# Performance work log

Measured on AMD Instinct MI355X. Metric: run time of the kernel, lower is better.

The kernel has to match this reference:

```python
import jax, jax.numpy as jnp
import numpy as np

K, D, N, W, OUT = 16, 2, 16384, 256, 1
TW = 0.2  # fixed_transition_width


def setup_inputs() -> dict:
    key = jax.random.key(0)
    ks = jax.random.split(key, 9)
    # 4x4 grid of subdomains over [0,1]^2
    edges = np.linspace(0.0, 1.0, 5).astype(np.float32)
    mins = np.array([[edges[i], edges[j]] for i in range(4) for j in range(4)], np.float32)
    maxs = mins + 0.25

    def init_w(k, shape, fan_in):
        return jax.random.normal(k, shape, jnp.float32) / np.sqrt(fan_in).astype(np.float32)

    return {
        "x": jax.random.uniform(ks[0], (N, D), jnp.float32),
        "W0": init_w(ks[1], (K, D, W), D),
        "b0": jnp.zeros((K, W), jnp.float32),
        "W1": init_w(ks[2], (K, W, W), W),
        "b1": jnp.zeros((K, W), jnp.float32),
        "W2": init_w(ks[3], (K, W, W), W),
        "b2": jnp.zeros((K, W), jnp.float32),
        "W3": init_w(ks[4], (K, W, OUT), W),
        "b3": jnp.zeros((K, OUT), jnp.float32),
        "xmins": jnp.asarray(mins),
        "xmaxs": jnp.asarray(maxs),
    }


def _cosine_window(xmins, xmaxs, wmin, x):
    """Normalized cosine partition-of-unity weights. x:[N,D], xmins/xmaxs:[K,D] -> [N,K]."""
    # smooth ramp 0->1 over [xmin-w, xmin+w] and 1->0 over [xmax-w, xmax+w], per dim
    t_l = jnp.clip((x[None] - (xmins - wmin)[:, None]) / (2.0 * wmin), 0.0, 1.0)  # [K,N,D]
    t_r = jnp.clip(((xmaxs + wmin)[:, None] - x[None]) / (2.0 * wmin), 0.0, 1.0)
    w_raw = jnp.prod(0.25 * (1.0 - jnp.cos(jnp.pi * t_l)) * (1.0 - jnp.cos(jnp.pi * t_r)), axis=-1)  # [K,N]
    w = w_raw / (jnp.sum(w_raw, axis=0, keepdims=True) + 1e-9)
    return w.T  # [N,K]


def reference(x, W0, b0, W1, b1, W2, b2, W3, b3, xmins, xmaxs):
    all_w = _cosine_window(xmins, xmaxs, TW, x)  # [N,K]
    # per-subdomain normalization of x to [-1,1]
    center = (xmins + xmaxs) * 0.5
    scale = jnp.maximum((xmaxs - xmins) * 0.5, 1e-9)
    xn = (x[None] - center[:, None]) / scale[:, None]  # [K,N,D]
    # batched small MLPs (one per subdomain), tanh hidden activations
    h = jnp.tanh(jnp.einsum('knd,kdw->knw', xn, W0) + b0[:, None])
    h = jnp.tanh(jnp.einsum('knw,kwv->knv', h, W1) + b1[:, None])
    h = jnp.tanh(jnp.einsum('knw,kwv->knv', h, W2) + b2[:, None])
    sub = jnp.einsum('knw,kwo->kno', h, W3) + b3[:, None]  # [K,N,OUT]
    # window-weighted combine; ansatz is identity in the NN output
    return jnp.einsum('nk,kno->no', all_w, sub)  # [N,OUT]
```

## Files before the change

kernel.cpp:

```cpp
#include <hip/hip_runtime.h>
#include <stdint.h>

#define TWF 0.2f
#define NPTS 16384

typedef __attribute__((ext_vector_type(8))) short short8;
typedef __attribute__((ext_vector_type(4))) float floatx4;

__device__ __forceinline__ short f2bf(float f){
  unsigned u = __float_as_uint(f);
  u += 0x7fff + ((u >> 16) & 1);
  return (short)(u >> 16);
}
__device__ __forceinline__ float bf2f(short s){
  return __uint_as_float(((unsigned)(unsigned short)s) << 16);
}
__device__ __forceinline__ float fast_tanh(float x){
  float e = __builtin_amdgcn_exp2f(x * 2.885390082f);
  float r = __builtin_amdgcn_rcpf(e + 1.f);
  return fmaf(-2.f, r, 1.f);
}
__device__ __forceinline__ float cospi_t(float t){
  return __builtin_amdgcn_cosf(t * 0.5f);
}
__device__ __forceinline__ unsigned cvt_pk_bf16(float lo, float hi){
  unsigned r;
  asm("v_cvt_pk_bf16_f32 %0, %1, %2" : "=v"(r) : "v"(lo), "v"(hi));
  return r;
}

#define WS_W      0
#define WS_REC    (4u<<20)
#define WS_CNT    (8u<<20)
#define CNT(k)    counts[(k) * 32]

__global__ __launch_bounds__(256) void prep_fused(
    const float* __restrict__ W1, const float* __restrict__ W2,
    const float* __restrict__ x,  const float* __restrict__ xmins,
    const float* __restrict__ xmaxs, short* __restrict__ dst,
    int* __restrict__ counts, floatx4* __restrict__ rec,
    float* __restrict__ out){
  if (blockIdx.x < 1024){
    int gid = blockIdx.x * 256 + threadIdx.x;
    int lane = gid & 63; int rest = gid >> 6;
    int jt = rest & 15; rest >>= 4;
    int ks = rest & 7;  rest >>= 3;
    int k  = rest & 15; int mat = rest >> 4;
    const float* W = mat ? W2 : W1;
    int j   = jt * 16 + (lane & 15);
    int kk0 = ks * 32 + (lane >> 4) * 8;
    short8 v;
    #pragma unroll
    for (int jj = 0; jj < 8; jj++)
      v[jj] = f2bf(W[k * 65536 + (kk0 + jj) * 256 + j]);
    *(short8*)(dst + (size_t)gid * 8) = v;
  } else {
    __shared__ int s_wrt[4][4];
    __shared__ int s_base;
    int b2   = blockIdx.x - 1024;
    int k    = b2 & 15;
    int cb   = (b2 >> 4) * 1024;
    int t    = threadIdx.x;
    int lane = t & 63, wave = t >> 6;

    float cx  = (xmins[k * 2 + 0] + xmaxs[k * 2 + 0]) * 0.5f;
    float cy  = (xmins[k * 2 + 1] + xmaxs[k * 2 + 1]) * 0.5f;
    float sxi = 1.f / fmaxf((xmaxs[k * 2 + 0] - xmins[k * 2 + 0]) * 0.5f, 1e-9f);
    float syi = 1.f / fmaxf((xmaxs[k * 2 + 1] - xmins[k * 2 + 1]) * 0.5f, 1e-9f);

    float pxr[4], pyr[4], sum[4], wk[4];
    #pragma unroll
    for (int r = 0; r < 4; r++){
      int p = cb + r * 256 + t;
      float2 xy = *(const float2*)&x[p * 2];
      pxr[r] = xy.x; pyr[r] = xy.y; sum[r] = 0.f; wk[r] = 0.f;
      if (k == 0) out[p] = 0.f;
    }
    #pragma unroll
    for (int kk = 0; kk < 16; kk++){
      float mnx = xmins[kk * 2 + 0], mny = xmins[kk * 2 + 1];
      float mxx = xmaxs[kk * 2 + 0], mxy = xmaxs[kk * 2 + 1];
      #pragma unroll
      for (int r = 0; r < 4; r++){
        float tlx = fminf(fmaxf((pxr[r] - (mnx - TWF)) * (1.f/(2.f*TWF)), 0.f), 1.f);
        float trx = fminf(fmaxf(((mxx + TWF) - pxr[r]) * (1.f/(2.f*TWF)), 0.f), 1.f);
        float tly = fminf(fmaxf((pyr[r] - (mny - TWF)) * (1.f/(2.f*TWF)), 0.f), 1.f);
        float tr2 = fminf(fmaxf(((mxy + TWF) - pyr[r]) * (1.f/(2.f*TWF)), 0.f), 1.f);
        float wx = 0.25f * (1.f - cospi_t(tlx)) * (1.f - cospi_t(trx));
        float wy = 0.25f * (1.f - cospi_t(tly)) * (1.f - cospi_t(tr2));
        float w  = wx * wy;
        sum[r] += w;
        if (kk == k) wk[r] = w;
      }
    }
    bool act[4]; float wn[4], xa[4], xb[4];
    unsigned long long msk[4]; int wtot[4];
    #pragma unroll
    for (int r = 0; r < 4; r++){
      float inv = 1.f / (sum[r] + 1e-9f);
      act[r] = wk[r] > 0.f;
      wn[r]  = wk[r] * inv;
      xa[r]  = (pxr[r] - cx) * sxi;
      xb[r]  = (pyr[r] - cy) * syi;
      msk[r] = __ballot(act[r]);
      wtot[r] = (int)__popcll(msk[r]);
    }
    if (lane == 0){
      #pragma unroll
      for (int r = 0; r < 4; r++) s_wrt[wave][r] = wtot[r];
    }
    __syncthreads();
    int wavebase = 0, blocktot = 0;
    #pragma unroll
    for (int w = 0; w < 4; w++){
      int ws_ = s_wrt[w][0] + s_wrt[w][1] + s_wrt[w][2] + s_wrt[w][3];
      blocktot += ws_;
      wavebase += (w < wave) ? ws_ : 0;
    }
    if (t == 0) s_base = atomicAdd(&CNT(k), blocktot);
    __syncthreads();
    int rb = 0;
    #pragma unroll
    for (int r = 0; r < 4; r++){
      if (act[r]){
        int pos = s_base + wavebase + rb +
                  (int)__popcll(msk[r] & ((1ull << lane) - 1ull));
        int p = cb + r * 256 + t;
        rec[k * NPTS + pos] = (floatx4){xa[r], xb[r], wn[r], __int_as_float(p)};
      }
      rb += s_wrt[wave][r];
    }
  }
}

__device__ __forceinline__ void store_h_packed(
    short* lds_h, const floatx4 (&acc)[4][4], const floatx4 (&bb)[4],
    int wave, int quad, int col){
  #pragma unroll
  for (int rt = 0; rt < 4; rt++){
    const int j0    = (wave * 4 + rt) * 16 + quad * 4;
    const int cbase = j0 >> 3;
    const int off   = j0 & 7;
    #pragma unroll
    for (int ct = 0; ct < 4; ct++){
      const int m = ct * 16 + col;
      float t0 = fast_tanh(acc[rt][ct][0] + bb[rt][0]);
      float t1 = fast_tanh(acc[rt][ct][1] + bb[rt][1]);
      float t2 = fast_tanh(acc[rt][ct][2] + bb[rt][2]);
      float t3 = fast_tanh(acc[rt][ct][3] + bb[rt][3]);
      uint2 v = make_uint2(cvt_pk_bf16(t0, t1), cvt_pk_bf16(t2, t3));
      *(uint2*)&lds_h[m * 256 + ((cbase ^ (m & 7)) << 3) + off] = v;
    }
  }
}

__global__ __launch_bounds__(256, 4) void fbpinn_main(
    const float* __restrict__ W0, const float* __restrict__ b0,
    const float* __restrict__ b1, const float* __restrict__ b2,
    const float* __restrict__ W3, const float* __restrict__ b3,
    const short* __restrict__ wsw, const int* __restrict__ counts,
    const floatx4* __restrict__ rec, float* __restrict__ out)
{
  __shared__ short lds_h[64 * 256];
  __shared__ float s_xn[64 * 2];
  __shared__ float s_win[64];
  __shared__ int   s_pidx[64];
  __shared__ float s_w3[256];
  __shared__ float s_w0[512];

  const int t    = threadIdx.x;
  const int lane = t & 63;
  const int wave = t >> 6;
  const int col  = lane & 15;
  const int quad = lane >> 4;

  int tb[17]; tb[0] = 0;
  #pragma unroll
  for (int kk = 0; kk < 16; kk++) tb[kk + 1] = tb[kk] + ((CNT(kk) + 63) >> 6);
  const int total = tb[16];

  const int xcd   = blockIdx.x & 7;
  const int nb    = gridDim.x >> 3;
  const int chunk = (total + 7) >> 3;

  for (int idx = blockIdx.x >> 3; idx < chunk; idx += nb){
    const int tile = xcd * chunk + idx;
    if (tile >= total) break;
    int k = 0;
    #pragma unroll
    for (int kk = 1; kk < 16; kk++) k += (tile >= tb[kk]);
    const int base = (tile - tb[k]) * 64;
    const int cnt  = CNT(k);

    __syncthreads();

    s_w3[t] = W3[k * 256 + t];
    s_w0[t] = W0[k * 512 + t];
    s_w0[256 + t] = W0[k * 512 + 256 + t];
    if (t < 64){
      int gi = base + t;
      bool valid = gi < cnt;
      floatx4 rc = rec[k * NPTS + (valid ? gi : 0)];
      s_pidx[t] = __float_as_int(rc[3]);
      s_win[t]  = valid ? rc[2] : 0.f;
      s_xn[t * 2 + 0] = rc[0];
      s_xn[t * 2 + 1] = rc[1];
    }
    __syncthreads();

    {
      short8 wfr[4], xfr[4];
      #pragma unroll
      for (int rt = 0; rt < 4; rt++){
        int j = (wave * 4 + rt) * 16 + col;
        short8 a;
        #pragma unroll
        for (int i = 0; i < 8; i++) a[i] = 0;
        a[0] = (quad == 0) ? f2bf(s_w0[j])       : (short)0;
        a[1] = (quad == 0) ? f2bf(s_w0[256 + j]) : (short)0;
        wfr[rt] = a;
      }
      #pragma unroll
      for (int ct = 0; ct < 4; ct++){
        int m = ct * 16 + col;
        short8 b;
        #pragma unroll
        for (int i = 0; i < 8; i++) b[i] = 0;
        b[0] = (quad == 0) ? f2bf(s_xn[m * 2 + 0]) : (short)0;
        b[1] = (quad == 0) ? f2bf(s_xn[m * 2 + 1]) : (short)0;
        xfr[ct] = b;
      }
      floatx4 bb[4];
      #pragma unroll
      for (int rt = 0; rt < 4; rt++)
        bb[rt] = *(const floatx4*)&b0[k * 256 + (wave * 4 + rt) * 16 + quad * 4];
      floatx4 acc[4][4];
      #pragma unroll
      for (int a = 0; a < 4; a++)
        #pragma unroll
        for (int b = 0; b < 4; b++)
          acc[a][b] = (floatx4){0.f, 0.f, 0.f, 0.f};
      #pragma unroll
      for (int rt = 0; rt < 4; rt++)
        #pragma unroll
        for (int ct = 0; ct < 4; ct++)
          acc[rt][ct] = __builtin_amdgcn_mfma_f32_16x16x32_bf16(wfr[rt], xfr[ct], acc[rt][ct], 0, 0, 0);
      store_h_packed(lds_h, acc, bb, wave, quad, col);
      __syncthreads();
    }

    #pragma unroll 1
    for (int layer = 0; layer < 2; layer++){
      const short8* wb = (const short8*)(wsw + (size_t)layer * 1048576)
                         + ((size_t)(k * 8) * 16 + wave * 4) * 64 + lane;
      const float*  bp = layer ? b2 : b1;
      floatx4 bb[4];
      #pragma unroll
      for (int rt = 0; rt < 4; rt++)
        bb[rt] = *(const floatx4*)&bp[k * 256 + (wave * 4 + rt) * 16 + quad * 4];
      floatx4 acc[4][4];
      #pragma unroll
      for (int a = 0; a < 4; a++)
        #pragma unroll
        for (int b = 0; b < 4; b++)
          acc[a][b] = (floatx4){0.f, 0.f, 0.f, 0.f};

      short8 wcur[4];
      #pragma unroll
      for (int rt = 0; rt < 4; rt++) wcur[rt] = wb[rt * 64];

      #pragma unroll
      for (int ks = 0; ks < 8; ks++){
        short8 wnxt[4];
        if (ks < 7){
          #pragma unroll
          for (int rt = 0; rt < 4; rt++)
            wnxt[rt] = wb[(ks + 1) * 1024 + rt * 64];
        }
        short8 hfr[4];
        #pragma unroll
        for (int ct = 0; ct < 4; ct++){
          int m   = ct * 16 + col;
          int pos = (ks * 4 + quad) ^ (m & 7);
          hfr[ct] = *(const short8*)&lds_h[m * 256 + pos * 8];
        }
        #pragma unroll
        for (int rt = 0; rt < 4; rt++)
          #pragma unroll
          for (int ct = 0; ct < 4; ct++)
            acc[rt][ct] = __builtin_amdgcn_mfma_f32_16x16x32_bf16(wcur[rt], hfr[ct], acc[rt][ct], 0, 0, 0);
        if (ks < 7){
          #pragma unroll
          for (int rt = 0; rt < 4; rt++) wcur[rt] = wnxt[rt];
        }
      }
      __syncthreads();

      store_h_packed(lds_h, acc, bb, wave, quad, col);
      __syncthreads();
    }

    {
      int m = t >> 2, q = t & 3;
      float dot = 0.f;
      #pragma unroll
      for (int cc = 0; cc < 8; cc++){
        int ci  = q * 8 + cc;
        int pos = ci ^ (m & 7);
        short8 hv = *(const short8*)&lds_h[m * 256 + pos * 8];
        #pragma unroll
        for (int jj = 0; jj < 8; jj++)
          dot = fmaf(bf2f(hv[jj]), s_w3[ci * 8 + jj], dot);
      }
      dot += __shfl_xor(dot, 1);
      dot += __shfl_xor(dot, 2);
      if (q == 0 && s_win[m] != 0.f)
        atomicAdd(&out[s_pidx[m]], s_win[m] * (dot + b3[k]));
    }
  }
}

extern "C" void kernel_launch(void* const* d_in, const int* in_sizes, int n_in,
                              void* d_out, int out_size, void* d_ws, size_t ws_size,
                              hipStream_t stream){
  const float* x     = (const float*)d_in[0];
  const float* W0    = (const float*)d_in[1];
  const float* b0    = (const float*)d_in[2];
  const float* W1    = (const float*)d_in[3];
  const float* b1    = (const float*)d_in[4];
  const float* W2    = (const float*)d_in[5];
  const float* b2    = (const float*)d_in[6];
  const float* W3    = (const float*)d_in[7];
  const float* b3    = (const float*)d_in[8];
  const float* xmins = (const float*)d_in[9];
  const float* xmaxs = (const float*)d_in[10];
  float* out = (float*)d_out;

  char* ws = (char*)d_ws;
  short*   wsw  = (short*)  (ws + WS_W);
  floatx4* rc   = (floatx4*)(ws + WS_REC);
  int*     cnts = (int*)    (ws + WS_CNT);

  (void)hipMemsetAsync(cnts, 0, 4096, stream);
  prep_fused<<<1024 + 256, 256, 0, stream>>>(W1, W2, x, xmins, xmaxs,
                                             wsw, cnts, rc, out);
  fbpinn_main<<<1024, 256, 0, stream>>>(W0, b0, b1, b2, W3, b3,
                                        wsw, cnts, rc, out);
}
```

Baseline: 148.1 us.

## Replace atomic counters and memset with per-chunk counts and in-kernel scan

The prep kernel now writes compaction counts per (subdomain, 1024-point chunk) segment without atomics. The separate memset launch goes away, and the window computation is folded into every fourth block of the weight-conversion grid. The main kernel builds a 256-entry prefix scan in LDS and binary-searches it to map each tile to its segment. This removes one launch and the global atomics. In exchange it adds partially filled tiles per chunk, which means more padded MFMA work, plus a scan and search in every block.

```diff
diff --git a/kernel.cpp b/kernel.cpp
--- a/kernel.cpp
+++ b/kernel.cpp
@@ -32,16 +32,28 @@
 #define WS_W      0
 #define WS_REC    (4u<<20)
 #define WS_CNT    (8u<<20)
-#define CNT(k)    counts[(k) * 32]
-
-__global__ __launch_bounds__(256) void prep_fused(
+
+struct SMem {
+  short lds_h[64 * 256];
+  float s_xn[64 * 2];
+  float s_win[64];
+  int   s_pidx[64];
+  float s_w3[256];
+  float s_w0[512];
+  int   s_stb[257];
+  int   s_c[256];
+};
+
+__global__ __launch_bounds__(256) void fbpinn_p0(
     const float* __restrict__ W1, const float* __restrict__ W2,
     const float* __restrict__ x,  const float* __restrict__ xmins,
     const float* __restrict__ xmaxs, short* __restrict__ dst,
-    int* __restrict__ counts, floatx4* __restrict__ rec,
-    float* __restrict__ out){
-  if (blockIdx.x < 1024){
-    int gid = blockIdx.x * 256 + threadIdx.x;
+    int* __restrict__ cnt, floatx4* __restrict__ rec, float* __restrict__ out)
+{
+  __shared__ int s_wrt[16];
+  const int bid = blockIdx.x, t = threadIdx.x;
+  int gid = bid * 256 + t;
+  {
     int lane = gid & 63; int rest = gid >> 6;
     int jt = rest & 15; rest >>= 4;
     int ks = rest & 7;  rest >>= 3;
@@ -54,82 +66,78 @@
     for (int jj = 0; jj < 8; jj++)
       v[jj] = f2bf(W[k * 65536 + (kk0 + jj) * 256 + j]);
     *(short8*)(dst + (size_t)gid * 8) = v;
-  } else {
-    __shared__ int s_wrt[4][4];
-    __shared__ int s_base;
-    int b2   = blockIdx.x - 1024;
-    int k    = b2 & 15;
-    int cb   = (b2 >> 4) * 1024;
-    int t    = threadIdx.x;
-    int lane = t & 63, wave = t >> 6;
-
-    float cx  = (xmins[k * 2 + 0] + xmaxs[k * 2 + 0]) * 0.5f;
-    float cy  = (xmins[k * 2 + 1] + xmaxs[k * 2 + 1]) * 0.5f;
-    float sxi = 1.f / fmaxf((xmaxs[k * 2 + 0] - xmins[k * 2 + 0]) * 0.5f, 1e-9f);
-    float syi = 1.f / fmaxf((xmaxs[k * 2 + 1] - xmins[k * 2 + 1]) * 0.5f, 1e-9f);
-
-    float pxr[4], pyr[4], sum[4], wk[4];
+  }
+  if (gid < NPTS) out[gid] = 0.f;
+
+  if ((bid & 3) != 0) return;
+  int L  = bid >> 2;
+  int k  = L & 15, ch = L >> 4;
+  int cb = ch * 1024;
+  int lane = t & 63, wave = t >> 6;
+
+  float cx  = (xmins[k * 2 + 0] + xmaxs[k * 2 + 0]) * 0.5f;
+  float cy  = (xmins[k * 2 + 1] + xmaxs[k * 2 + 1]) * 0.5f;
+  float sxi = 1.f / fmaxf((xmaxs[k * 2 + 0] - xmins[k * 2 + 0]) * 0.5f, 1e-9f);
+  float syi = 1.f / fmaxf((xmaxs[k * 2 + 1] - xmins[k * 2 + 1]) * 0.5f, 1e-9f);
+
+  float pxr[4], pyr[4], sum[4], wk[4];
+  #pragma unroll
+  for (int r = 0; r < 4; r++){
+    int p = cb + r * 256 + t;
+    float2 xy = *(const float2*)&x[p * 2];
+    pxr[r] = xy.x; pyr[r] = xy.y; sum[r] = 0.f; wk[r] = 0.f;
+  }
+  #pragma unroll
+  for (int kk = 0; kk < 16; kk++){
+    float mnx = xmins[kk * 2 + 0], mny = xmins[kk * 2 + 1];
+    float mxx = xmaxs[kk * 2 + 0], mxy = xmaxs[kk * 2 + 1];
     #pragma unroll
     for (int r = 0; r < 4; r++){
+      float tlx = fminf(fmaxf((pxr[r] - (mnx - TWF)) * (1.f/(2.f*TWF)), 0.f), 1.f);
+      float trx = fminf(fmaxf(((mxx + TWF) - pxr[r]) * (1.f/(2.f*TWF)), 0.f), 1.f);
+      float tly = fminf(fmaxf((pyr[r] - (mny - TWF)) * (1.f/(2.f*TWF)), 0.f), 1.f);
+      float tr2 = fminf(fmaxf(((mxy + TWF) - pyr[r]) * (1.f/(2.f*TWF)), 0.f), 1.f);
+      float wx = 0.25f * (1.f - cospi_t(tlx)) * (1.f - cospi_t(trx));
+      float wy = 0.25f * (1.f - cospi_t(tly)) * (1.f - cospi_t(tr2));
+      float w  = wx * wy;
+      sum[r] += w;
+      if (kk == k) wk[r] = w;
+    }
+  }
+  bool act[4]; float wn[4], xa[4], xb[4];
+  unsigned long long msk[4]; int wtot[4];
+  #pragma unroll
+  for (int r = 0; r < 4; r++){
+    float inv = 1.f / (sum[r] + 1e-9f);
+    act[r] = wk[r] > 0.f;
+    wn[r]  = wk[r] * inv;
+    xa[r]  = (pxr[r] - cx) * sxi;
+    xb[r]  = (pyr[r] - cy) * syi;
+    msk[r] = __ballot(act[r]);
+    wtot[r] = (int)__popcll(msk[r]);
+  }
+  if (lane == 0){
+    #pragma unroll
+    for (int r = 0; r < 4; r++) s_wrt[wave * 4 + r] = wtot[r];
+  }
+  __syncthreads();
+  int wavebase = 0, blocktot = 0;
+  #pragma unroll
+  for (int w = 0; w < 4; w++){
+    int ws_ = s_wrt[w*4+0] + s_wrt[w*4+1] + s_wrt[w*4+2] + s_wrt[w*4+3];
+    blocktot += ws_;
+    wavebase += (w < wave) ? ws_ : 0;
+  }
+  if (t == 0) cnt[k * 16 + ch] = blocktot;
+  int rb = 0;
+  #pragma unroll
+  for (int r = 0; r < 4; r++){
+    if (act[r]){
+      int pos = wavebase + rb + (int)__popcll(msk[r] & ((1ull << lane) - 1ull));
       int p = cb + r * 256 + t;
-      float2 xy = *(const float2*)&x[p * 2];
-      pxr[r] = xy.x; pyr[r] = xy.y; sum[r] = 0.f; wk[r] = 0.f;
-      if (k == 0) out[p] = 0.f;
-    }
-    #pragma unroll
-    for (int kk = 0; kk < 16; kk++){
-      float mnx = xmins[kk * 2 + 0], mny = xmins[kk * 2 + 1];
-      float mxx = xmaxs[kk * 2 + 0], mxy = xmaxs[kk * 2 + 1];
-      #pragma unroll
-      for (int r = 0; r < 4; r++){
-        float tlx = fminf(fmaxf((pxr[r] - (mnx - TWF)) * (1.f/(2.f*TWF)), 0.f), 1.f);
-        float trx = fminf(fmaxf(((mxx + TWF) - pxr[r]) * (1.f/(2.f*TWF)), 0.f), 1.f);
-        float tly = fminf(fmaxf((pyr[r] - (mny - TWF)) * (1.f/(2.f*TWF)), 0.f), 1.f);
-        float tr2 = fminf(fmaxf(((mxy + TWF) - pyr[r]) * (1.f/(2.f*TWF)), 0.f), 1.f);
-        float wx = 0.25f * (1.f - cospi_t(tlx)) * (1.f - cospi_t(trx));
-        float wy = 0.25f * (1.f - cospi_t(tly)) * (1.f - cospi_t(tr2));
-        float w  = wx * wy;
-        sum[r] += w;
-        if (kk == k) wk[r] = w;
-      }
-    }
-    bool act[4]; float wn[4], xa[4], xb[4];
-    unsigned long long msk[4]; int wtot[4];
-    #pragma unroll
-    for (int r = 0; r < 4; r++){
-      float inv = 1.f / (sum[r] + 1e-9f);
-      act[r] = wk[r] > 0.f;
-      wn[r]  = wk[r] * inv;
-      xa[r]  = (pxr[r] - cx) * sxi;
-      xb[r]  = (pyr[r] - cy) * syi;
-      msk[r] = __ballot(act[r]);
-      wtot[r] = (int)__popcll(msk[r]);
-    }
-    if (lane == 0){
-      #pragma unroll
-      for (int r = 0; r < 4; r++) s_wrt[wave][r] = wtot[r];
-    }
-    __syncthreads();
-    int wavebase = 0, blocktot = 0;
-    #pragma unroll
-    for (int w = 0; w < 4; w++){
-      int ws_ = s_wrt[w][0] + s_wrt[w][1] + s_wrt[w][2] + s_wrt[w][3];
-      blocktot += ws_;
-      wavebase += (w < wave) ? ws_ : 0;
-    }
-    if (t == 0) s_base = atomicAdd(&CNT(k), blocktot);
-    __syncthreads();
-    int rb = 0;
-    #pragma unroll
-    for (int r = 0; r < 4; r++){
-      if (act[r]){
-        int pos = s_base + wavebase + rb +
-                  (int)__popcll(msk[r] & ((1ull << lane) - 1ull));
-        int p = cb + r * 256 + t;
-        rec[k * NPTS + pos] = (floatx4){xa[r], xb[r], wn[r], __int_as_float(p)};
-      }
-      rb += s_wrt[wave][r];
-    }
+      rec[k * NPTS + cb + pos] = (floatx4){xa[r], xb[r], wn[r], __int_as_float(p)};
+    }
+    rb += s_wrt[wave * 4 + r];
   }
 }
 
@@ -154,57 +162,64 @@
   }
 }
 
-__global__ __launch_bounds__(256, 4) void fbpinn_main(
+__global__ __launch_bounds__(256, 4) void fbpinn_p1(
     const float* __restrict__ W0, const float* __restrict__ b0,
     const float* __restrict__ b1, const float* __restrict__ b2,
     const float* __restrict__ W3, const float* __restrict__ b3,
-    const short* __restrict__ wsw, const int* __restrict__ counts,
+    const short* __restrict__ wsw, const int* __restrict__ cnt,
     const floatx4* __restrict__ rec, float* __restrict__ out)
 {
-  __shared__ short lds_h[64 * 256];
-  __shared__ float s_xn[64 * 2];
-  __shared__ float s_win[64];
-  __shared__ int   s_pidx[64];
-  __shared__ float s_w3[256];
-  __shared__ float s_w0[512];
-
-  const int t    = threadIdx.x;
+  __shared__ SMem sm;
+  const int bid  = blockIdx.x, t = threadIdx.x;
   const int lane = t & 63;
   const int wave = t >> 6;
   const int col  = lane & 15;
   const int quad = lane >> 4;
 
-  int tb[17]; tb[0] = 0;
-  #pragma unroll
-  for (int kk = 0; kk < 16; kk++) tb[kk + 1] = tb[kk] + ((CNT(kk) + 63) >> 6);
-  const int total = tb[16];
-
-  const int xcd   = blockIdx.x & 7;
-  const int nb    = gridDim.x >> 3;
-  const int chunk = (total + 7) >> 3;
-
-  for (int idx = blockIdx.x >> 3; idx < chunk; idx += nb){
-    const int tile = xcd * chunk + idx;
+  int* s_scan = (int*)sm.lds_h;
+  if (t < 256){ int c = cnt[t]; sm.s_c[t] = c; s_scan[t] = (c + 63) >> 6; }
+  __syncthreads();
+  for (int off = 1; off < 256; off <<= 1){
+    int v = (t >= off) ? s_scan[t - off] : 0;
+    __syncthreads();
+    s_scan[t] += v;
+    __syncthreads();
+  }
+  if (t < 256) sm.s_stb[t + 1] = s_scan[t];
+  if (t == 0)  sm.s_stb[0] = 0;
+  __syncthreads();
+  const int total = sm.s_stb[256];
+
+  const int xcd    = bid & 7;
+  const int nb     = gridDim.x >> 3;
+  const int chunkT = (total + 7) >> 3;
+
+  for (int idx = bid >> 3; idx < chunkT; idx += nb){
+    const int tile = xcd * chunkT + idx;
     if (tile >= total) break;
-    int k = 0;
-    #pragma unroll
-    for (int kk = 1; kk < 16; kk++) k += (tile >= tb[kk]);
-    const int base = (tile - tb[k]) * 64;
-    const int cnt  = CNT(k);
+    int lo = 0, hi = 256;
+    while (hi - lo > 1){
+      int mid = (lo + hi) >> 1;
+      if (tile >= sm.s_stb[mid]) lo = mid; else hi = mid;
+    }
+    const int seg = lo, k = seg >> 4, ch = seg & 15;
+    const int c     = sm.s_c[seg];
+    const int lbase = (tile - sm.s_stb[seg]) * 64;
+    const floatx4* rbase = rec + k * NPTS + ch * 1024;
 
     __syncthreads();
 
-    s_w3[t] = W3[k * 256 + t];
-    s_w0[t] = W0[k * 512 + t];
-    s_w0[256 + t] = W0[k * 512 + 256 + t];
+    sm.s_w3[t] = W3[k * 256 + t];
+    sm.s_w0[t] = W0[k * 512 + t];
+    sm.s_w0[256 + t] = W0[k * 512 + 256 + t];
     if (t < 64){
-      int gi = base + t;
-      bool valid = gi < cnt;
-      floatx4 rc = rec[k * NPTS + (valid ? gi : 0)];
-      s_pidx[t] = __float_as_int(rc[3]);
-      s_win[t]  = valid ? rc[2] : 0.f;
-      s_xn[t * 2 + 0] = rc[0];
-      s_xn[t * 2 + 1] = rc[1];
+      int li = lbase + t;
+      bool valid = li < c;
+      floatx4 rcd = rbase[valid ? li : 0];
+      sm.s_pidx[t] = __float_as_int(rcd[3]);
+      sm.s_win[t]  = valid ? rcd[2] : 0.f;
+      sm.s_xn[t * 2 + 0] = rcd[0];
+      sm.s_xn[t * 2 + 1] = rcd[1];
     }
     __syncthreads();
 
@@ -216,8 +231,8 @@
         short8 a;
         #pragma unroll
         for (int i = 0; i < 8; i++) a[i] = 0;
-        a[0] = (quad == 0) ? f2bf(s_w0[j])       : (short)0;
-        a[1] = (quad == 0) ? f2bf(s_w0[256 + j]) : (short)0;
+        a[0] = (quad == 0) ? f2bf(sm.s_w0[j])       : (short)0;
+        a[1] = (quad == 0) ? f2bf(sm.s_w0[256 + j]) : (short)0;
         wfr[rt] = a;
       }
       #pragma unroll
@@ -226,8 +241,8 @@
         short8 b;
         #pragma unroll
         for (int i = 0; i < 8; i++) b[i] = 0;
-        b[0] = (quad == 0) ? f2bf(s_xn[m * 2 + 0]) : (short)0;
-        b[1] = (quad == 0) ? f2bf(s_xn[m * 2 + 1]) : (short)0;
+        b[0] = (quad == 0) ? f2bf(sm.s_xn[m * 2 + 0]) : (short)0;
+        b[1] = (quad == 0) ? f2bf(sm.s_xn[m * 2 + 1]) : (short)0;
         xfr[ct] = b;
       }
       floatx4 bb[4];
@@ -245,7 +260,7 @@
         #pragma unroll
         for (int ct = 0; ct < 4; ct++)
           acc[rt][ct] = __builtin_amdgcn_mfma_f32_16x16x32_bf16(wfr[rt], xfr[ct], acc[rt][ct], 0, 0, 0);
-      store_h_packed(lds_h, acc, bb, wave, quad, col);
+      store_h_packed(sm.lds_h, acc, bb, wave, quad, col);
       __syncthreads();
     }
 
@@ -282,7 +297,7 @@
         for (int ct = 0; ct < 4; ct++){
           int m   = ct * 16 + col;
           int pos = (ks * 4 + quad) ^ (m & 7);
-          hfr[ct] = *(const short8*)&lds_h[m * 256 + pos * 8];
+          hfr[ct] = *(const short8*)&sm.lds_h[m * 256 + pos * 8];
         }
         #pragma unroll
         for (int rt = 0; rt < 4; rt++)
@@ -296,7 +311,7 @@
       }
       __syncthreads();
 
-      store_h_packed(lds_h, acc, bb, wave, quad, col);
+      store_h_packed(sm.lds_h, acc, bb, wave, quad, col);
       __syncthreads();
     }
 
@@ -307,15 +322,15 @@
       for (int cc = 0; cc < 8; cc++){
         int ci  = q * 8 + cc;
         int pos = ci ^ (m & 7);
-        short8 hv = *(const short8*)&lds_h[m * 256 + pos * 8];
+        short8 hv = *(const short8*)&sm.lds_h[m * 256 + pos * 8];
         #pragma unroll
         for (int jj = 0; jj < 8; jj++)
-          dot = fmaf(bf2f(hv[jj]), s_w3[ci * 8 + jj], dot);
+          dot = fmaf(bf2f(hv[jj]), sm.s_w3[ci * 8 + jj], dot);
       }
       dot += __shfl_xor(dot, 1);
       dot += __shfl_xor(dot, 2);
-      if (q == 0 && s_win[m] != 0.f)
-        atomicAdd(&out[s_pidx[m]], s_win[m] * (dot + b3[k]));
+      if (q == 0 && sm.s_win[m] != 0.f)
+        atomicAdd(&out[sm.s_pidx[m]], sm.s_win[m] * (dot + b3[k]));
     }
   }
 }
@@ -338,12 +353,11 @@
 
   char* ws = (char*)d_ws;
   short*   wsw  = (short*)  (ws + WS_W);
-  floatx4* rc   = (floatx4*)(ws + WS_REC);
-  int*     cnts = (int*)    (ws + WS_CNT);
-
-  (void)hipMemsetAsync(cnts, 0, 4096, stream);
-  prep_fused<<<1024 + 256, 256, 0, stream>>>(W1, W2, x, xmins, xmaxs,
-                                             wsw, cnts, rc, out);
-  fbpinn_main<<<1024, 256, 0, stream>>>(W0, b0, b1, b2, W3, b3,
-                                        wsw, cnts, rc, out);
-}
+  floatx4* rec  = (floatx4*)(ws + WS_REC);
+  int*     cnt  = (int*)    (ws + WS_CNT);
+
+  fbpinn_p0<<<1024, 256, 0, stream>>>(W1, W2, x, xmins, xmaxs,
+                                      wsw, cnt, rec, out);
+  fbpinn_p1<<<1024, 256, 0, stream>>>(W0, b0, b1, b2, W3, b3,
+                                      wsw, cnt, rec, out);
+}
```

Result: slower. 153.6 us (+3.7%).
